# Kernel optimization log

Hardware: AMD Instinct MI355X
Metric: run time of the kernel (lower is better)

The kernel has to match this reference:

```python
import jax, jax.numpy as jnp
import numpy as np

N = 100000
E = 1600000

def _gc(x, W, b, src, tgt, w):
    # GraphConvolution: transform, gather per-edge messages from src,
    # weight by the sparse aggregation matrix entries (Mtgt values),
    # scatter-sum into target nodes, add bias.
    support = x @ W                       # [N, out]
    msg = support[src] * w[:, None]        # [E, out]
    agg = jax.ops.segment_sum(msg, tgt, num_segments=N)  # [N, out]
    return agg + b

def setup_inputs() -> dict:
    key = jax.random.key(0)
    ks = jax.random.split(key, 10)
    d_in, d_h, d_out = 128, 64, 40
    x = jax.random.normal(ks[0], (N, d_in), dtype=jnp.float32)
    src = jax.random.randint(ks[1], (E,), 0, N)
    tgt = jax.random.randint(ks[2], (E,), 0, N)
    mtgt_w = jax.random.uniform(ks[3], (E,), dtype=jnp.float32)
    def glorot(k, shape):
        lim = 1.0 / np.sqrt(shape[0])
        return jax.random.uniform(k, shape, jnp.float32, -lim, lim)
    return {
        'x': x, 'src': src, 'tgt': tgt, 'mtgt_w': mtgt_w,
        'W0': glorot(ks[4], (d_in, d_h)), 'b0': jnp.zeros((d_h,), jnp.float32),
        'W1': glorot(ks[5], (d_h, d_h)),  'b1': jnp.zeros((d_h,), jnp.float32),
        'W2': glorot(ks[6], (d_h, d_h)),  'b2': jnp.zeros((d_h,), jnp.float32),
        'W3': glorot(ks[7], (d_h, d_out)),'b3': jnp.zeros((d_out,), jnp.float32),
    }

def reference(x, src, tgt, mtgt_w, W0, b0, W1, b1, W2, b2, W3, b3):
    # RESK forward, eval mode (dropout = identity), nlayers=4, residue_layers=1.
    h = jax.nn.relu(_gc(x, W0, b0, src, tgt, mtgt_w))
    # middle layer 1: residual block (r = h; h = relu(gc(h)) + r)
    r = h
    h = jax.nn.relu(_gc(h, W1, b1, src, tgt, mtgt_w)) + r
    # middle layer 2: residual block
    r = h
    h = jax.nn.relu(_gc(h, W2, b2, src, tgt, mtgt_w)) + r
    out = _gc(h, W3, b3, src, tgt, mtgt_w)
    return jax.nn.log_softmax(out, axis=1)
```

## Files before the change

kernel.cpp:

```cpp
#include <hip/hip_runtime.h>
#include <cstdint>
#include <cstddef>
#include <math.h>


typedef unsigned int uint;
typedef unsigned short ushort;
typedef unsigned char uchar;

typedef __attribute__((ext_vector_type(8))) short bf16x8;
typedef __attribute__((ext_vector_type(4))) float f32x4;

constexpr int NB_ROWS = 256;
constexpr int CHUNK   = 2048;
constexpr int CAP     = 4608;

__device__ __forceinline__ uint f2bf(float f) {
    uint u = __float_as_uint(f);
    return (u + 0x7FFFu + ((u >> 16) & 1u)) >> 16;
}

__global__ void zero_ints(int* __restrict__ p, int n) {
    int i = blockIdx.x * blockDim.x + threadIdx.x;
    if (i < n) p[i] = 0;
}

__global__ void prep_wt(const float* __restrict__ W0, const float* __restrict__ W1,
                        const float* __restrict__ W2, const float* __restrict__ W3,
                        ushort* __restrict__ wt0, ushort* __restrict__ wt1,
                        ushort* __restrict__ wt2, ushort* __restrict__ wt3) {
    int i = blockIdx.x * 256 + threadIdx.x;
    if (i < 64 * 128) {
        int c = i >> 7, k = i & 127;
        wt0[i] = (ushort)f2bf(W0[k * 64 + c]);
    }
    if (i < 64 * 64) {
        int c = i >> 6, k = i & 63;
        wt1[i] = (ushort)f2bf(W1[k * 64 + c]);
        wt2[i] = (ushort)f2bf(W2[k * 64 + c]);
        wt3[i] = (c < 40) ? (ushort)f2bf(W3[k * 40 + c]) : (ushort)0;
    }
}

__global__ __launch_bounds__(512) void bucket_kernel(const int* __restrict__ src,
                                                     const int* __restrict__ tgt,
                                                     const float* __restrict__ w,
                                                     int* __restrict__ bcur,
                                                     uint* __restrict__ bkt,
                                                     uchar* __restrict__ brow,
                                                     int E, int NB) {
    __shared__ uint binned[CHUNK];
    __shared__ ushort binb[CHUNK];
    __shared__ uchar binr[CHUNK];
    __shared__ int hist[512];
    __shared__ int sc[512];
    __shared__ int cur[512];
    __shared__ int gbase[512];
    int tid = threadIdx.x;
    int e0 = blockIdx.x * CHUNK;
    int cnt = min(CHUNK, E - e0);
    hist[tid] = 0;
    __syncthreads();
    for (int i = tid; i < cnt; i += 512) atomicAdd(&hist[tgt[e0 + i] >> 8], 1);
    __syncthreads();
    int v = hist[tid];
    sc[tid] = v;
    __syncthreads();
    for (int off = 1; off < 512; off <<= 1) {
        int t = (tid >= off) ? sc[tid - off] : 0;
        __syncthreads();
        sc[tid] += t;
        __syncthreads();
    }
    int excl = sc[tid] - v;
    if (tid < NB && v > 0) gbase[tid] = atomicAdd(&bcur[tid], v);
    __syncthreads();
    hist[tid] = excl;
    cur[tid] = excl;
    __syncthreads();
    for (int i = tid; i < cnt; i += 512) {
        int t = tgt[e0 + i];
        int b = t >> 8;
        int r = atomicAdd(&cur[b], 1);
        float wf = w[e0 + i];
        uint w15 = (uint)(int)(wf * 32767.f + 0.5f);
        if (w15 > 32767u) w15 = 32767u;
        binned[r] = (uint)src[e0 + i] | (w15 << 17);
        binb[r] = (ushort)b;
        binr[r] = (uchar)(t & 255);
    }
    __syncthreads();
    for (int i = tid; i < cnt; i += 512) {
        int b = binb[i];
        int dst = gbase[b] + (i - hist[b]);
        if (dst < CAP) {
            bkt[(size_t)b * CAP + dst] = binned[i];
            brow[(size_t)b * CAP + dst] = binr[i];
        }
    }
}

__global__ void bscan_kernel(const int* __restrict__ bcur, int* __restrict__ bbase,
                             int* __restrict__ row_start, int NB, int N) {
    __shared__ int sd[512];
    int tid = threadIdx.x;
    int tot = (tid < NB) ? min(bcur[tid], CAP) : 0;
    sd[tid] = tot;
    __syncthreads();
    for (int off = 1; off < 512; off <<= 1) {
        int t = (tid >= off) ? sd[tid - off] : 0;
        __syncthreads();
        sd[tid] += t;
        __syncthreads();
    }
    if (tid < NB) bbase[tid] = sd[tid] - tot;
    if (tid == 511) row_start[N] = sd[511];
}

__global__ __launch_bounds__(1024) void rowsort_kernel(const uint* __restrict__ bkt,
                                                       const uchar* __restrict__ brow,
                                                       const int* __restrict__ bcur,
                                                       const int* __restrict__ bbase,
                                                       uint* __restrict__ csr,
                                                       int* __restrict__ row_start, int N) {
    __shared__ int hist[256];
    __shared__ int offs[256];
    int b = blockIdx.x;
    int tid = threadIdx.x;
    int cnt = min(bcur[b], CAP);
    const uint* win = bkt + (size_t)b * CAP;
    const uchar* wrow = brow + (size_t)b * CAP;
    if (tid < 256) hist[tid] = 0;
    __syncthreads();
    uint en[5];
    uchar er[5];
    int ne = 0;
#pragma unroll
    for (int k = 0; k < 5; ++k) {
        int i = tid + k * 1024;
        if (i < cnt) {
            en[k] = win[i];
            er[k] = wrow[i];
            atomicAdd(&hist[er[k]], 1);
            ne = k + 1;
        }
    }
    __syncthreads();
    int v = 0;
    if (tid < 256) { v = hist[tid]; offs[tid] = v; }
    __syncthreads();
    for (int off = 1; off < 256; off <<= 1) {
        int t = 0;
        if (tid < 256 && tid >= off) t = offs[tid - off];
        __syncthreads();
        if (tid < 256) offs[tid] += t;
        __syncthreads();
    }
    int gb = bbase[b];
    if (tid < 256) {
        int excl = offs[tid] - v;
        int row = (b << 8) + tid;
        if (row < N) row_start[row] = gb + excl;
        hist[tid] = excl;
    }
    __syncthreads();
#pragma unroll
    for (int k = 0; k < 5; ++k) {
        if (k < ne) {
            int pos = atomicAdd(&hist[er[k]], 1);
            csr[gb + pos] = en[k];
        }
    }
}

template <int K>
__global__ __launch_bounds__(256) void gemm_mfma(const float* __restrict__ H,
                                                 const ushort* __restrict__ Wt,
                                                 uint* __restrict__ out, int n) {
    constexpr int NT = K / 32;
    __shared__ ushort alds[64 * K];
    int tid = threadIdx.x;
    int nbase = blockIdx.x * 64;
    int rows = min(64, n - nbase);

    const float4* Hg = (const float4*)(H + (size_t)nbase * K);
#pragma unroll
    for (int it = 0; it < K / 16; ++it) {
        int i = tid + it * 256;
        int r = i / (K / 4);
        int c4 = i % (K / 4);
        if (r < rows) {
            float4 v = Hg[i];
            uint2 pk;
            pk.x = f2bf(v.x) | (f2bf(v.y) << 16);
            pk.y = f2bf(v.z) | (f2bf(v.w) << 16);
            uint bcol = ((uint)(c4 * 8)) ^ (((uint)(r & 7)) << 4);
            *(uint2*)((char*)alds + r * (K * 2) + bcol) = pk;
        }
    }

    int wv = __builtin_amdgcn_readfirstlane(tid >> 6);
    int l = tid & 63;
    int lr = l & 15;
    int lh = l >> 4;

    bf16x8 wf[4][NT];
#pragma unroll
    for (int ct = 0; ct < 4; ++ct)
#pragma unroll
        for (int ks = 0; ks < NT; ++ks)
            wf[ct][ks] = *(const bf16x8*)(const void*)(Wt + (ct * 16 + lr) * K + ks * 32 + lh * 8);

    __syncthreads();

    f32x4 acc[4];
#pragma unroll
    for (int ct = 0; ct < 4; ++ct) acc[ct] = (f32x4){0.f, 0.f, 0.f, 0.f};

    int row = wv * 16 + lr;
#pragma unroll
    for (int ks = 0; ks < NT; ++ks) {
        uint bcol = ((uint)(ks * 64 + lh * 16)) ^ (((uint)(row & 7)) << 4);
        bf16x8 hf = *(const bf16x8*)((const char*)alds + row * (K * 2) + bcol);
#pragma unroll
        for (int ct = 0; ct < 4; ++ct)
            acc[ct] = __builtin_amdgcn_mfma_f32_16x16x32_bf16(wf[ct][ks], hf, acc[ct], 0, 0, 0);
    }

    int node = nbase + row;
    if (node < n) {
        uint* orow = out + (size_t)node * 32;
#pragma unroll
        for (int ct = 0; ct < 4; ++ct) {
            uint2 pk;
            pk.x = f2bf(acc[ct][0]) | (f2bf(acc[ct][1]) << 16);
            pk.y = f2bf(acc[ct][2]) | (f2bf(acc[ct][3]) << 16);
            *(uint2*)(orow + ct * 8 + lh * 2) = pk;
        }
    }
}

__device__ __forceinline__ float wval(uint d) {
    return (float)(d >> 17) * (1.0f / 32767.f);
}

__device__ __forceinline__ float blo(uint u) { return __uint_as_float(u << 16); }
__device__ __forceinline__ float bhi(uint u) { return __uint_as_float(u & 0xFFFF0000u); }

__global__ __launch_bounds__(256) void agg64_kernel(const ushort* __restrict__ sb,
                                                    const int* __restrict__ row_start,
                                                    const uint* __restrict__ csr,
                                                    const float* __restrict__ bias,
                                                    const float* __restrict__ resid,
                                                    float* __restrict__ out, int n) {
    int wid = (blockIdx.x * blockDim.x + threadIdx.x) >> 6;
    int lane = threadIdx.x & 63;
    if (wid >= n) return;
    int q = lane >> 4;
    int c = lane & 15;
    int beg = __builtin_amdgcn_readfirstlane(row_start[wid]);
    int end = __builtin_amdgcn_readfirstlane(row_start[wid + 1]);
    float a0 = 0.f, a1 = 0.f, a2 = 0.f, a3 = 0.f;
    uint voff = (uint)(c << 3);
    for (int e0 = beg; e0 < end; e0 += 64) {
        int ei = e0 + lane;
        uint mye = (ei < end) ? csr[ei] : 0u;
        int m = end - e0;
        if (m > 64) m = 64;
        for (int eb = 0; eb < m; eb += 16) {
            uint dd[4];
#pragma unroll
            for (int k = 0; k < 4; ++k)
                dd[k] = (uint)__builtin_amdgcn_ds_bpermute((eb + 4 * k + q) << 2, (int)mye);
            uint2 uu[4];
#pragma unroll
            for (int k = 0; k < 4; ++k) {
                uint off = ((dd[k] & 0x1FFFFu) << 7) | voff;
                uu[k] = *(const uint2*)((const char*)sb + off);
            }
#pragma unroll
            for (int k = 0; k < 4; ++k) {
                float wv = wval(dd[k]);
                a0 = fmaf(blo(uu[k].x), wv, a0);
                a1 = fmaf(bhi(uu[k].x), wv, a1);
                a2 = fmaf(blo(uu[k].y), wv, a2);
                a3 = fmaf(bhi(uu[k].y), wv, a3);
            }
        }
    }
    a0 += __shfl_xor(a0, 16); a1 += __shfl_xor(a1, 16);
    a2 += __shfl_xor(a2, 16); a3 += __shfl_xor(a3, 16);
    a0 += __shfl_xor(a0, 32); a1 += __shfl_xor(a1, 32);
    a2 += __shfl_xor(a2, 32); a3 += __shfl_xor(a3, 32);
    if (lane < 16) {
        float4 bv = *(const float4*)(bias + 4 * c);
        float h0 = fmaxf(a0 + bv.x, 0.f);
        float h1 = fmaxf(a1 + bv.y, 0.f);
        float h2 = fmaxf(a2 + bv.z, 0.f);
        float h3 = fmaxf(a3 + bv.w, 0.f);
        if (resid) {
            float4 rv = *(const float4*)(resid + (size_t)wid * 64 + 4 * c);
            h0 += rv.x;
            h1 += rv.y;
            h2 += rv.z;
            h3 += rv.w;
        }
        *(float4*)(out + (size_t)wid * 64 + 4 * c) = make_float4(h0, h1, h2, h3);
    }
}

__global__ __launch_bounds__(256) void agg_final_kernel(const ushort* __restrict__ sb,
                                                        const int* __restrict__ row_start,
                                                        const uint* __restrict__ csr,
                                                        const float* __restrict__ bias,
                                                        float* __restrict__ out, int n) {
    int wid = (blockIdx.x * blockDim.x + threadIdx.x) >> 6;
    int lane = threadIdx.x & 63;
    if (wid >= n) return;
    int q = lane >> 4;
    int c = lane & 15;
    int beg = __builtin_amdgcn_readfirstlane(row_start[wid]);
    int end = __builtin_amdgcn_readfirstlane(row_start[wid + 1]);
    float a0 = 0.f, a1 = 0.f, a2 = 0.f, a3 = 0.f;
    uint voff = (uint)(c << 3);
    for (int e0 = beg; e0 < end; e0 += 64) {
        int ei = e0 + lane;
        uint mye = (ei < end) ? csr[ei] : 0u;
        int m = end - e0;
        if (m > 64) m = 64;
        for (int eb = 0; eb < m; eb += 16) {
            uint dd[4];
#pragma unroll
            for (int k = 0; k < 4; ++k)
                dd[k] = (uint)__builtin_amdgcn_ds_bpermute((eb + 4 * k + q) << 2, (int)mye);
            uint2 uu[4];
#pragma unroll
            for (int k = 0; k < 4; ++k) {
                uint off = ((dd[k] & 0x1FFFFu) << 7) | voff;
                uu[k] = *(const uint2*)((const char*)sb + off);
            }
#pragma unroll
            for (int k = 0; k < 4; ++k) {
                float wv = wval(dd[k]);
                a0 = fmaf(blo(uu[k].x), wv, a0);
                a1 = fmaf(bhi(uu[k].x), wv, a1);
                a2 = fmaf(blo(uu[k].y), wv, a2);
                a3 = fmaf(bhi(uu[k].y), wv, a3);
            }
        }
    }
    a0 += __shfl_xor(a0, 16); a1 += __shfl_xor(a1, 16);
    a2 += __shfl_xor(a2, 16); a3 += __shfl_xor(a3, 16);
    a0 += __shfl_xor(a0, 32); a1 += __shfl_xor(a1, 32);
    a2 += __shfl_xor(a2, 32); a3 += __shfl_xor(a3, 32);
    bool act = c < 10;
    float v0 = -INFINITY, v1 = -INFINITY, v2 = -INFINITY, v3 = -INFINITY;
    if (act) {
        float4 bv = *(const float4*)(bias + 4 * c);
        v0 = a0 + bv.x;
        v1 = a1 + bv.y;
        v2 = a2 + bv.z;
        v3 = a3 + bv.w;
    }
    float m = fmaxf(fmaxf(v0, v1), fmaxf(v2, v3));
#pragma unroll
    for (int d = 1; d < 16; d <<= 1) m = fmaxf(m, __shfl_xor(m, d));
    float ex = act ? (expf(v0 - m) + expf(v1 - m) + expf(v2 - m) + expf(v3 - m)) : 0.f;
#pragma unroll
    for (int d = 1; d < 16; d <<= 1) ex += __shfl_xor(ex, d);
    float lse = m + logf(ex);
    if (act && lane < 16)
        *(float4*)(out + (size_t)wid * 40 + 4 * c) =
            make_float4(v0 - lse, v1 - lse, v2 - lse, v3 - lse);
}

extern "C" void kernel_launch(void* const* d_in, const int* in_sizes, int n_in,
                              void* d_out, int out_size, void* d_ws, size_t ws_size,
                              hipStream_t stream) {
    const float* x   = (const float*)d_in[0];
    const int*   src = (const int*)d_in[1];
    const int*   tgt = (const int*)d_in[2];
    const float* mw  = (const float*)d_in[3];
    const float* W0  = (const float*)d_in[4];
    const float* b0  = (const float*)d_in[5];
    const float* W1  = (const float*)d_in[6];
    const float* b1  = (const float*)d_in[7];
    const float* W2  = (const float*)d_in[8];
    const float* b2  = (const float*)d_in[9];
    const float* W3  = (const float*)d_in[10];
    const float* b3  = (const float*)d_in[11];
    float* out = (float*)d_out;

    const int N = in_sizes[0] / 128;
    const int E = in_sizes[1];
    const int NB = (N + NB_ROWS - 1) / NB_ROWS;

    char* p = (char*)d_ws;
    auto carve = [&](size_t bytes) {
        char* r = p;
        p += (bytes + 255) & ~size_t(255);
        return r;
    };
    int*    bcur      = (int*)carve((size_t)NB * 4);
    int*    bbase     = (int*)carve((size_t)NB * 4);
    int*    row_start = (int*)carve((size_t)(N + 1) * 4);
    uint*   bkt       = (uint*)carve((size_t)NB * CAP * 4);
    uchar*  brow      = (uchar*)carve((size_t)NB * CAP);
    uint*   csr       = (uint*)carve((size_t)E * 4);
    ushort* support   = (ushort*)carve((size_t)N * 64 * 2);
    float*  h         = (float*)carve((size_t)N * 64 * 4);
    ushort* wt0       = (ushort*)carve((size_t)64 * 128 * 2);
    ushort* wt1       = (ushort*)carve((size_t)64 * 64 * 2);
    ushort* wt2       = (ushort*)carve((size_t)64 * 64 * 2);
    ushort* wt3       = (ushort*)carve((size_t)64 * 64 * 2);

    int gblocks = (N + 63) / 64;
    int ablocks = (N + 3) / 4;

    zero_ints<<<(NB + 255) / 256, 256, 0, stream>>>(bcur, NB);
    prep_wt<<<32, 256, 0, stream>>>(W0, W1, W2, W3, wt0, wt1, wt2, wt3);
    bucket_kernel<<<(E + CHUNK - 1) / CHUNK, 512, 0, stream>>>(src, tgt, mw, bcur, bkt, brow, E, NB);
    bscan_kernel<<<1, 512, 0, stream>>>(bcur, bbase, row_start, NB, N);
    rowsort_kernel<<<NB, 1024, 0, stream>>>(bkt, brow, bcur, bbase, csr, row_start, N);

    gemm_mfma<128><<<gblocks, 256, 0, stream>>>(x, wt0, (uint*)support, N);
    agg64_kernel<<<ablocks, 256, 0, stream>>>(support, row_start, csr, b0, nullptr, h, N);
    gemm_mfma<64><<<gblocks, 256, 0, stream>>>(h, wt1, (uint*)support, N);
    agg64_kernel<<<ablocks, 256, 0, stream>>>(support, row_start, csr, b1, h, h, N);
    gemm_mfma<64><<<gblocks, 256, 0, stream>>>(h, wt2, (uint*)support, N);
    agg64_kernel<<<ablocks, 256, 0, stream>>>(support, row_start, csr, b2, h, h, N);
    gemm_mfma<64><<<gblocks, 256, 0, stream>>>(h, wt3, (uint*)support, N);
    agg_final_kernel<<<ablocks, 256, 0, stream>>>(support, row_start, csr, b3, out, N);
}
```

Before: 389.7 us.

## Aggregate four nodes per wavefront with one quarter-wave per node

The aggregation kernels now assign four consecutive target nodes to each 64-lane wavefront, with each 16-lane group owning one node, instead of one node per wavefront split across four edge streams. Edge entries for all four nodes are loaded cooperatively in 64-wide windows and broadcast with bpermute, which removes the cross-group shuffle reduction and cuts the per-node wavefront count by four. The cost is load imbalance: groups whose node has fewer edges idle while the wave loops to the group maximum, and each group now processes edges serially four at a time.

```diff
diff --git a/kernel.cpp b/kernel.cpp
--- a/kernel.cpp
+++ b/kernel.cpp
@@ -247,6 +247,59 @@
 __device__ __forceinline__ float blo(uint u) { return __uint_as_float(u << 16); }
 __device__ __forceinline__ float bhi(uint u) { return __uint_as_float(u & 0xFFFF0000u); }
 
+__device__ __forceinline__ void agg4_body(const ushort* __restrict__ sb,
+                                          const int* __restrict__ row_start,
+                                          const uint* __restrict__ csr, int n0,
+                                          int lane, int N, float& a0, float& a1,
+                                          float& a2, float& a3) {
+    int g = lane >> 4;
+    uint voff = (uint)((lane & 15) << 3);
+    const char* sbc = (const char*)sb;
+
+    int idx = n0 + lane;
+    if (idx > N) idx = N;
+    int rsv = (lane <= 4) ? row_start[idx] : 0;
+    int rs0 = __shfl(rsv, 0);
+    int myb = __shfl(rsv, g);
+    int mye = __shfl(rsv, g + 1);
+    int tend = __shfl(rsv, 4);
+
+    for (int W0 = rs0; W0 < tend; W0 += 64) {
+        int ei = W0 + lane;
+        uint entry = (ei < tend) ? csr[ei] : 0u;
+        int lo = myb - W0;
+        if (lo < 0) lo = 0;
+        int hi = mye - W0;
+        if (hi > 64) hi = 64;
+        int cnt = hi - lo;
+        if (cnt < 0) cnt = 0;
+        int mx = cnt;
+        mx = max(mx, __shfl_xor(mx, 16));
+        mx = max(mx, __shfl_xor(mx, 32));
+        for (int o = 0; o < mx; o += 4) {
+            uint dd[4];
+            uint2 uu[4];
+#pragma unroll
+            for (int j = 0; j < 4; ++j) {
+                int p = (lo + o + j) & 63;
+                uint d = (uint)__builtin_amdgcn_ds_bpermute(p << 2, (int)entry);
+                dd[j] = ((o + j) < cnt) ? d : 0u;
+            }
+#pragma unroll
+            for (int j = 0; j < 4; ++j)
+                uu[j] = *(const uint2*)(sbc + (((dd[j] & 0x1FFFFu) << 7) | voff));
+#pragma unroll
+            for (int j = 0; j < 4; ++j) {
+                float wv = wval(dd[j]);
+                a0 = fmaf(blo(uu[j].x), wv, a0);
+                a1 = fmaf(bhi(uu[j].x), wv, a1);
+                a2 = fmaf(blo(uu[j].y), wv, a2);
+                a3 = fmaf(bhi(uu[j].y), wv, a3);
+            }
+        }
+    }
+}
+
 __global__ __launch_bounds__(256) void agg64_kernel(const ushort* __restrict__ sb,
                                                     const int* __restrict__ row_start,
                                                     const uint* __restrict__ csr,
@@ -255,57 +308,27 @@
                                                     float* __restrict__ out, int n) {
     int wid = (blockIdx.x * blockDim.x + threadIdx.x) >> 6;
     int lane = threadIdx.x & 63;
-    if (wid >= n) return;
-    int q = lane >> 4;
+    int n0 = wid * 4;
+    if (n0 >= n) return;
+    float a0 = 0.f, a1 = 0.f, a2 = 0.f, a3 = 0.f;
+    agg4_body(sb, row_start, csr, n0, lane, n, a0, a1, a2, a3);
+    int g = lane >> 4;
     int c = lane & 15;
-    int beg = __builtin_amdgcn_readfirstlane(row_start[wid]);
-    int end = __builtin_amdgcn_readfirstlane(row_start[wid + 1]);
-    float a0 = 0.f, a1 = 0.f, a2 = 0.f, a3 = 0.f;
-    uint voff = (uint)(c << 3);
-    for (int e0 = beg; e0 < end; e0 += 64) {
-        int ei = e0 + lane;
-        uint mye = (ei < end) ? csr[ei] : 0u;
-        int m = end - e0;
-        if (m > 64) m = 64;
-        for (int eb = 0; eb < m; eb += 16) {
-            uint dd[4];
-#pragma unroll
-            for (int k = 0; k < 4; ++k)
-                dd[k] = (uint)__builtin_amdgcn_ds_bpermute((eb + 4 * k + q) << 2, (int)mye);
-            uint2 uu[4];
-#pragma unroll
-            for (int k = 0; k < 4; ++k) {
-                uint off = ((dd[k] & 0x1FFFFu) << 7) | voff;
-                uu[k] = *(const uint2*)((const char*)sb + off);
-            }
-#pragma unroll
-            for (int k = 0; k < 4; ++k) {
-                float wv = wval(dd[k]);
-                a0 = fmaf(blo(uu[k].x), wv, a0);
-                a1 = fmaf(bhi(uu[k].x), wv, a1);
-                a2 = fmaf(blo(uu[k].y), wv, a2);
-                a3 = fmaf(bhi(uu[k].y), wv, a3);
-            }
-        }
-    }
-    a0 += __shfl_xor(a0, 16); a1 += __shfl_xor(a1, 16);
-    a2 += __shfl_xor(a2, 16); a3 += __shfl_xor(a3, 16);
-    a0 += __shfl_xor(a0, 32); a1 += __shfl_xor(a1, 32);
-    a2 += __shfl_xor(a2, 32); a3 += __shfl_xor(a3, 32);
-    if (lane < 16) {
+    int nd = n0 + g;
+    if (nd < n) {
         float4 bv = *(const float4*)(bias + 4 * c);
         float h0 = fmaxf(a0 + bv.x, 0.f);
         float h1 = fmaxf(a1 + bv.y, 0.f);
         float h2 = fmaxf(a2 + bv.z, 0.f);
         float h3 = fmaxf(a3 + bv.w, 0.f);
         if (resid) {
-            float4 rv = *(const float4*)(resid + (size_t)wid * 64 + 4 * c);
+            float4 rv = *(const float4*)(resid + (size_t)nd * 64 + 4 * c);
             h0 += rv.x;
             h1 += rv.y;
             h2 += rv.z;
             h3 += rv.w;
         }
-        *(float4*)(out + (size_t)wid * 64 + 4 * c) = make_float4(h0, h1, h2, h3);
+        *(float4*)(out + (size_t)nd * 64 + 4 * c) = make_float4(h0, h1, h2, h3);
     }
 }
 
@@ -316,43 +339,13 @@
                                                         float* __restrict__ out, int n) {
     int wid = (blockIdx.x * blockDim.x + threadIdx.x) >> 6;
     int lane = threadIdx.x & 63;
-    if (wid >= n) return;
-    int q = lane >> 4;
+    int n0 = wid * 4;
+    if (n0 >= n) return;
+    float a0 = 0.f, a1 = 0.f, a2 = 0.f, a3 = 0.f;
+    agg4_body(sb, row_start, csr, n0, lane, n, a0, a1, a2, a3);
+    int g = lane >> 4;
     int c = lane & 15;
-    int beg = __builtin_amdgcn_readfirstlane(row_start[wid]);
-    int end = __builtin_amdgcn_readfirstlane(row_start[wid + 1]);
-    float a0 = 0.f, a1 = 0.f, a2 = 0.f, a3 = 0.f;
-    uint voff = (uint)(c << 3);
-    for (int e0 = beg; e0 < end; e0 += 64) {
-        int ei = e0 + lane;
-        uint mye = (ei < end) ? csr[ei] : 0u;
-        int m = end - e0;
-        if (m > 64) m = 64;
-        for (int eb = 0; eb < m; eb += 16) {
-            uint dd[4];
-#pragma unroll
-            for (int k = 0; k < 4; ++k)
-                dd[k] = (uint)__builtin_amdgcn_ds_bpermute((eb + 4 * k + q) << 2, (int)mye);
-            uint2 uu[4];
-#pragma unroll
-            for (int k = 0; k < 4; ++k) {
-                uint off = ((dd[k] & 0x1FFFFu) << 7) | voff;
-                uu[k] = *(const uint2*)((const char*)sb + off);
-            }
-#pragma unroll
-            for (int k = 0; k < 4; ++k) {
-                float wv = wval(dd[k]);
-                a0 = fmaf(blo(uu[k].x), wv, a0);
-                a1 = fmaf(bhi(uu[k].x), wv, a1);
-                a2 = fmaf(blo(uu[k].y), wv, a2);
-                a3 = fmaf(bhi(uu[k].y), wv, a3);
-            }
-        }
-    }
-    a0 += __shfl_xor(a0, 16); a1 += __shfl_xor(a1, 16);
-    a2 += __shfl_xor(a2, 16); a3 += __shfl_xor(a3, 16);
-    a0 += __shfl_xor(a0, 32); a1 += __shfl_xor(a1, 32);
-    a2 += __shfl_xor(a2, 32); a3 += __shfl_xor(a3, 32);
+    int nd = n0 + g;
     bool act = c < 10;
     float v0 = -INFINITY, v1 = -INFINITY, v2 = -INFINITY, v3 = -INFINITY;
     if (act) {
@@ -369,8 +362,8 @@
 #pragma unroll
     for (int d = 1; d < 16; d <<= 1) ex += __shfl_xor(ex, d);
     float lse = m + logf(ex);
-    if (act && lane < 16)
-        *(float4*)(out + (size_t)wid * 40 + 4 * c) =
+    if (act && nd < n)
+        *(float4*)(out + (size_t)nd * 40 + 4 * c) =
             make_float4(v0 - lse, v1 - lse, v2 - lse, v3 - lse);
 }
 
@@ -415,7 +408,7 @@
     ushort* wt3       = (ushort*)carve((size_t)64 * 64 * 2);
 
     int gblocks = (N + 63) / 64;
-    int ablocks = (N + 3) / 4;
+    int ablocks = (N + 15) / 16;
 
     zero_ints<<<(NB + 255) / 256, 256, 0, stream>>>(bcur, NB);
     prep_wt<<<32, 256, 0, stream>>>(W0, W1, W2, W3, wt0, wt1, wt2, wt3);
```

Result: faster. 356.2 us (-8.6%).
